# Kernel optimization log

Measured on AMD Instinct MI355X. Metric: run time of the kernel, lower is better.

The kernel has to match this reference:

```python
import jax, jax.numpy as jnp
import numpy as np

H = 1024; W = 1024
SPACE_SIGMA = 16.0; RANGE_SIGMA = 0.25
PAD_XY = 2; PAD_Z = 2
DIM = 5


def setup_inputs() -> dict:
    key = jax.random.key(0)
    k1, k2 = jax.random.split(key)
    features = jax.random.uniform(k1, (H, W, 3), dtype=jnp.float32)
    inp = jax.random.normal(k2, (H, W, 3), dtype=jnp.float32)
    return {"features": features, "inp": inp}


def _grid_dims(features_np):
    # Grid sizes are data-dependent in the original (TF builds them from
    # per-channel min/max); compute them host-side from concrete inputs.
    sh = int(float(H - 1) / SPACE_SIGMA) + 1 + 2 * PAD_XY
    sw = int(float(W - 1) / SPACE_SIGMA) + 1 + 2 * PAD_XY
    depths = []
    for c in range(3):
        ch = features_np[..., c]
        delta = float(ch.max() - ch.min())
        depths.append(int(delta / RANGE_SIGMA) + 1 + 2 * PAD_Z)
    return (sh, sw, depths[0], depths[1], depths[2])


def _both_indices(size, coord):
    left = jnp.clip(coord.astype(jnp.int32), 0, size - 1)
    right = jnp.clip(left + 1, 0, size - 1)
    return left, right


def _convn(data, n_iter=2):
    # Faithful port of the TF convn: separable [1,2,1]/4 pass per axis with
    # the exact same ping-pong buffer / boundary-keep / transpose behavior.
    buffer = jnp.zeros_like(data)
    perm = (1, 2, 3, 4, 0)
    for _ in range(n_iter):
        buffer, data = data, buffer
        for _ in range(DIM):
            newdata = (buffer[:-2] + buffer[2:] + 2.0 * buffer[1:-1]) / 4.0
            data = jnp.concatenate([data[:1], newdata, data[-1:]], axis=0)
            data = jnp.transpose(data, perm)
            buffer = jnp.transpose(buffer, perm)
    return data


def _filter(features, inp, dims):
    sh, sw, dr, dg, db = dims
    hw = H * W
    yy, xx = jnp.meshgrid(jnp.arange(H, dtype=jnp.float32),
                          jnp.arange(W, dtype=jnp.float32), indexing="ij")
    splat_yy = (yy / SPACE_SIGMA + 0.5).astype(jnp.int32) + PAD_XY
    splat_xx = (xx / SPACE_SIGMA + 0.5).astype(jnp.int32) + PAD_XY
    slice_yy = yy / SPACE_SIGMA + PAD_XY
    slice_xx = xx / SPACE_SIGMA + PAD_XY
    y_i, y_i2 = _both_indices(sh, slice_yy)
    x_i, x_i2 = _both_indices(sw, slice_xx)
    y_alpha = (slice_yy - y_i.astype(jnp.float32)).reshape(-1)
    x_alpha = (slice_xx - x_i.astype(jnp.float32)).reshape(-1)

    chans = []
    for c, depth in zip(range(3), (dr, dg, db)):
        v = features[..., c]
        v0 = v - jnp.min(v)
        splat_v = (v0 / RANGE_SIGMA + 0.5).astype(jnp.int32) + PAD_Z
        slice_v = v0 / RANGE_SIGMA + PAD_Z
        li, ri = _both_indices(depth, slice_v)
        alpha = (slice_v - li.astype(jnp.float32)).reshape(-1)
        chans.append((splat_v, li, ri, alpha))
    (splat_rr, r_i, r_i2, r_alpha) = chans[0]
    (splat_gg, g_i, g_i2, g_alpha) = chans[1]
    (splat_bb, b_i, b_i2, b_alpha) = chans[2]

    splat_coords = ((((splat_yy * sw + splat_xx) * dr + splat_rr) * dg
                     + splat_gg) * db + splat_bb).reshape(-1)  # [hw]

    idx_all = jnp.stack([y_i, y_i2, x_i, x_i2, r_i, r_i2,
                         g_i, g_i2, b_i, b_i2]).reshape(10, hw)
    alphas_all = jnp.stack([1.0 - y_alpha, y_alpha, 1.0 - x_alpha, x_alpha,
                            1.0 - r_alpha, r_alpha, 1.0 - g_alpha, g_alpha,
                            1.0 - b_alpha, b_alpha])  # [10, hw]

    # 32 corners of the 5-D hypercube; sel[c, d] picks left/right index per dim.
    corners = np.stack(np.meshgrid(*([np.arange(2)] * DIM), indexing="ij"),
                       axis=-1).reshape(-1, DIM)
    sel = corners + np.arange(DIM) * 2  # [32, 5]

    strides = (sw, dr, dg, db)
    coord = idx_all[sel[:, 0]]  # [32, hw]
    for d in range(1, DIM):
        coord = coord * strides[d - 1] + idx_all[sel[:, d]]
    alpha_prod = alphas_all[sel[:, 0]]  # [32, hw]
    for d in range(1, DIM):
        alpha_prod = alpha_prod * alphas_all[sel[:, d]]

    total = sh * sw * dr * dg * db

    def ch_filter(ch):
        grid = jnp.zeros((total,), jnp.float32).at[splat_coords].add(ch.reshape(-1))
        grid = _convn(grid.reshape(sh, sw, dr, dg, db))
        vals = grid.reshape(-1)[coord]  # [32, hw] multilinear gather
        return jnp.sum(alpha_prod * vals, axis=0).reshape(H, W)

    outT = jax.vmap(ch_filter)(jnp.transpose(inp, (2, 0, 1)))
    return jnp.transpose(outT, (1, 2, 0))


def reference(features, inp):
    dims = _grid_dims(np.asarray(features))
    return _filter(features, inp, dims)
```

## Files before the change

kernel.cpp:

```cpp
#include <hip/hip_runtime.h>

namespace {

constexpr int kH  = 1024;
constexpr int kW  = 1024;
constexpr int kHW = kH * kW;
constexpr int kSH = 68;
constexpr int kSW = 68;
constexpr int kD  = 8;
constexpr int kT3 = kSH * kSW * kD * kD * kD;

__global__ void minmax_kernel(const float* __restrict__ feat, float* __restrict__ part) {
    const float4* f4 = (const float4*)feat;
    float mn[3] = {1e30f, 1e30f, 1e30f};
    float mx[3] = {-1e30f, -1e30f, -1e30f};
    int tid = blockIdx.x * blockDim.x + threadIdx.x;
    int stride = gridDim.x * blockDim.x;
    for (int c = tid; c < kHW / 4; c += stride) {
        float4 q0 = f4[c * 3], q1 = f4[c * 3 + 1], q2 = f4[c * 3 + 2];
        mn[0] = fminf(mn[0], fminf(fminf(q0.x, q0.w), fminf(q1.z, q2.y)));
        mx[0] = fmaxf(mx[0], fmaxf(fmaxf(q0.x, q0.w), fmaxf(q1.z, q2.y)));
        mn[1] = fminf(mn[1], fminf(fminf(q0.y, q1.x), fminf(q1.w, q2.z)));
        mx[1] = fmaxf(mx[1], fmaxf(fmaxf(q0.y, q1.x), fmaxf(q1.w, q2.z)));
        mn[2] = fminf(mn[2], fminf(fminf(q0.z, q1.y), fminf(q2.x, q2.w)));
        mx[2] = fmaxf(mx[2], fmaxf(fmaxf(q0.z, q1.y), fmaxf(q2.x, q2.w)));
    }
    #pragma unroll
    for (int off = 32; off > 0; off >>= 1) {
        #pragma unroll
        for (int c = 0; c < 3; ++c) {
            mn[c] = fminf(mn[c], __shfl_down(mn[c], off, 64));
            mx[c] = fmaxf(mx[c], __shfl_down(mx[c], off, 64));
        }
    }
    __shared__ float smn[4][3], smx[4][3];
    int wave = threadIdx.x >> 6;
    if ((threadIdx.x & 63) == 0) {
        #pragma unroll
        for (int c = 0; c < 3; ++c) { smn[wave][c] = mn[c]; smx[wave][c] = mx[c]; }
    }
    __syncthreads();
    if (threadIdx.x == 0) {
        #pragma unroll
        for (int c = 0; c < 3; ++c) {
            part[blockIdx.x * 6 + c]     = fminf(fminf(smn[0][c], smn[1][c]), fminf(smn[2][c], smn[3][c]));
            part[blockIdx.x * 6 + 3 + c] = fmaxf(fmaxf(smx[0][c], smx[1][c]), fmaxf(smx[2][c], smx[3][c]));
        }
    }
}

__global__ void params_kernel(const float* __restrict__ part, float* __restrict__ hdrF) {
    int t = threadIdx.x;
    float mn[3], mx[3];
    #pragma unroll
    for (int c = 0; c < 3; ++c) { mn[c] = part[t * 6 + c]; mx[c] = part[t * 6 + 3 + c]; }
    #pragma unroll
    for (int off = 32; off > 0; off >>= 1) {
        #pragma unroll
        for (int c = 0; c < 3; ++c) {
            mn[c] = fminf(mn[c], __shfl_down(mn[c], off, 64));
            mx[c] = fmaxf(mx[c], __shfl_down(mx[c], off, 64));
        }
    }
    __shared__ float smn[4][3], smx[4][3];
    int wave = t >> 6;
    if ((t & 63) == 0) {
        #pragma unroll
        for (int c = 0; c < 3; ++c) { smn[wave][c] = mn[c]; smx[wave][c] = mx[c]; }
    }
    __syncthreads();
    if (t == 0) {
        int* ip = (int*)(hdrF + 8);
        #pragma unroll
        for (int c = 0; c < 3; ++c) {
            float bmn = fminf(fminf(smn[0][c], smn[1][c]), fminf(smn[2][c], smn[3][c]));
            float bmx = fmaxf(fmaxf(smx[0][c], smx[1][c]), fmaxf(smx[2][c], smx[3][c]));
            float delta = bmx - bmn;
            int depth = (int)((double)delta / 0.25) + 1 + 4;
            if (depth > kD) depth = kD;
            if (depth < 1) depth = 1;
            hdrF[c] = bmn;
            ip[c] = depth;
        }
    }
}

__global__ __launch_bounds__(256) void splat_kernel(const float* __restrict__ feat,
                                                    const float* __restrict__ inp,
                                                    const float* __restrict__ hdrF,
                                                    float* __restrict__ grid) {
    int ix = blockIdx.x, iy = blockIdx.y;
    int y0 = (iy == 0) ? 0 : 16 * iy - 8;
    int x0 = (ix == 0) ? 0 : 16 * ix - 8;
    int h = (iy == 0 || iy == 64) ? 8 : 16;
    int w = (ix == 0 || ix == 64) ? 8 : 16;

    __shared__ float acc[3 * 512];
    __shared__ float fS[16 * 48], iS[16 * 48];
    for (int i = threadIdx.x; i < 3 * 512; i += 256) acc[i] = 0.0f;

    int rowVec = (w * 3) >> 2;
    int nvec = h * rowVec;
    const float4* f4 = (const float4*)(feat + ((long)y0 * kW + x0) * 3);
    const float4* i4 = (const float4*)(inp  + ((long)y0 * kW + x0) * 3);
    for (int t = threadIdx.x; t < nvec; t += 256) {
        int row = t / rowVec, q = t - row * rowVec;
        ((float4*)fS)[row * rowVec + q] = f4[row * (kW * 3 / 4) + q];
        ((float4*)iS)[row * rowVec + q] = i4[row * (kW * 3 / 4) + q];
    }
    __syncthreads();

    int t = threadIdx.x;
    int n = w * h;
    if (t < n) {
        int lx = t & (w - 1);
        int ly = (w == 16) ? (t >> 4) : (t >> 3);
        int o = (ly * w + lx) * 3;
        float v0 = fS[o + 0] - hdrF[0];
        float v1 = fS[o + 1] - hdrF[1];
        float v2 = fS[o + 2] - hdrF[2];
        int sr = (int)(v0 * 4.0f + 0.5f) + 2;
        int sg = (int)(v1 * 4.0f + 0.5f) + 2;
        int sb = (int)(v2 * 4.0f + 0.5f) + 2;
        int ci = (sr << 6) + (sg << 3) + sb;
        atomicAdd(&acc[ci],        iS[o + 0]);
        atomicAdd(&acc[512 + ci],  iS[o + 1]);
        atomicAdd(&acc[1024 + ci], iS[o + 2]);
    }
    __syncthreads();

    long base = ((long)((iy + 2) * kSW + (ix + 2))) << 9;
    for (int i = threadIdx.x; i < 512; i += 256) {
        int b = i >> 6, r = (i >> 3) & 7, g = i & 7;
        int s = (r << 6) + (g << 3) + b;
        grid[base + i]            = acc[s];
        grid[kT3 + base + i]      = acc[512 + s];
        grid[2 * kT3 + base + i]  = acc[1024 + s];
    }
}

__global__ __launch_bounds__(192) void blur2_kernel(float* __restrict__ dst,
                                                    const float* __restrict__ src,
                                                    const float* __restrict__ hdrF) {
    int cx = blockIdx.x + 2, cy = blockIdx.y + 2;
    const int* ip = (const int*)(hdrF + 8);
    int dr = ip[0], dg = ip[1], db = ip[2];

    __shared__ float Sv[3 * 576];
    long cbase = ((long)(cy * kSW + cx)) << 9;

    {
        const float4* g4 = (const float4*)src;
        for (int i = threadIdx.x; i < 384; i += 192) {
            int ch = i >> 7, i4 = i & 127;
            float4 q = g4[(long)ch * (kT3 / 4) + (cbase >> 2) + i4];
            int b = i4 >> 4;
            int rg = ((i4 >> 1) & 7) * 8 + (i4 & 1) * 4;
            *(float4*)&Sv[ch * 576 + b * 72 + rg] = q;
        }
    }
    __syncthreads();

    int ch = threadIdx.x >> 6;
    int rg = threadIdx.x & 63;
    int r = rg >> 3, g = rg & 7;

    float* S = Sv + ch * 576;
    auto SV = [&](int b, int l) -> float { return S[b * 72 + l]; };
    auto gsp = [&](int ccy, int ccx, int rr, int gg, int bb) -> float {
        if (ccy < 2 || ccy > 66 || ccx < 2 || ccx > 66) return 0.0f;
        return src[(long)ch * kT3 + (((long)(ccy * kSW + ccx)) << 9) + (bb << 6) + (rr << 3) + gg];
    };

    bool gI = (g >= 1) && (g <= dg - 2);
    bool rI = (r >= 1) && (r <= dr - 2);

    float v[8];
    #pragma unroll
    for (int b = 0; b < 8; ++b) v[b] = SV(b, rg);

    int eHi = db - 1;

    auto o1_end = [&](int e) -> float {
        float Vm, Vp;
        if (gI)      { Vm = SV(e, rg - 1); Vp = SV(e, rg + 1); }
        else if (rI) { Vm = SV(e, rg - 8); Vp = SV(e, rg + 8); }
        else         { Vm = gsp(cy, cx - 1, r, g, e); Vp = gsp(cy, cx + 1, r, g, e); }
        return (Vm + Vp + 2.0f * SV(e, rg)) * 0.25f;
    };
    float o1_lo = o1_end(0);
    float o1_hi = o1_end(eHi);

    float o1[8];
    #pragma unroll
    for (int b = 0; b < 8; ++b) {
        float iv = 0.0f;
        if (b >= 1 && b <= 6) iv = ((v[b - 1] + v[b + 1]) + 2.0f * v[b]) * 0.25f;
        o1[b] = (b >= 1 && b <= db - 2) ? iv : (b == 0 ? o1_lo : (b == eHi ? o1_hi : 0.0f));
    }

    auto out1_in = [&](int r2, int g2, int e) -> float {
        int l2 = (r2 << 3) + g2;
        float C = SV(e, l2);
        float Nm, Np;
        if (g2 >= 1 && g2 <= dg - 2)      { Nm = SV(e, l2 - 1); Np = SV(e, l2 + 1); }
        else if (r2 >= 1 && r2 <= dr - 2) { Nm = SV(e, l2 - 8); Np = SV(e, l2 + 8); }
        else { Nm = gsp(cy, cx - 1, r2, g2, e); Np = gsp(cy, cx + 1, r2, g2, e); }
        return (Nm + Np + 2.0f * C) * 0.25f;
    };
    auto out1_x = [&](int cx2, int e) -> float {
        float C = gsp(cy, cx2, r, g, e);
        float Nm, Np;
        if (cx2 >= 1 && cx2 <= kSW - 2) { Nm = gsp(cy, cx2 - 1, r, g, e); Np = gsp(cy, cx2 + 1, r, g, e); }
        else                            { Nm = gsp(cy - 1, cx2, r, g, e); Np = gsp(cy + 1, cx2, r, g, e); }
        return (Nm + Np + 2.0f * C) * 0.25f;
    };
    auto o2_end = [&](int e, float o1e) -> float {
        float Xm, Xp;
        if (gI)      { Xm = out1_in(r, g - 1, e); Xp = out1_in(r, g + 1, e); }
        else if (rI) { Xm = out1_in(r - 1, g, e); Xp = out1_in(r + 1, g, e); }
        else         { Xm = out1_x(cx - 1, e);    Xp = out1_x(cx + 1, e); }
        return (Xm + Xp + 2.0f * o1e) * 0.25f;
    };
    float o2_lo = o2_end(0, o1_lo);
    float o2_hi = o2_end(eHi, o1_hi);

    float o2[8];
    #pragma unroll
    for (int b = 0; b < 8; ++b) {
        float iv = 0.0f;
        if (b >= 1 && b <= 6) iv = ((o1[b - 1] + o1[b + 1]) + 2.0f * o1[b]) * 0.25f;
        o2[b] = (b >= 1 && b <= db - 2) ? iv : (b == 0 ? o2_lo : (b == eHi ? o2_hi : 0.0f));
    }

    float* dp = dst + (long)ch * kT3 + cbase + (rg << 3);
    *(float4*)dp       = make_float4(o2[0], o2[1], o2[2], o2[3]);
    *(float4*)(dp + 4) = make_float4(o2[4], o2[5], o2[6], o2[7]);
}

__global__ __launch_bounds__(256) void slice_kernel(const float* __restrict__ feat,
                                                    const float* __restrict__ hdrF,
                                                    const float* __restrict__ grid,
                                                    float* __restrict__ out) {
    __shared__ float sg[3 * 4 * 512 + 8];
    int tx = blockIdx.x, ty = blockIdx.y;

    {
        const float4* g4 = (const float4*)grid;
        float4* s4 = (float4*)sg;
        #pragma unroll
        for (int it = 0; it < 2; ++it) {
            int i = threadIdx.x + it * 256;
            int cell = i >> 7;
            int ci4 = i & 127;
            int cy = ty + 2 + (cell >> 1), cx = tx + 2 + (cell & 1);
            long cbase4 = ((long)(cy * kSW + cx)) << 7;
            #pragma unroll
            for (int ch = 0; ch < 3; ++ch)
                s4[ch * 512 + i] = g4[(long)ch * (kT3 / 4) + cbase4 + ci4];
        }
    }
    __syncthreads();

    const int* ip = (const int*)(hdrF + 8);
    int d3[3] = {ip[0], ip[1], ip[2]};
    int lx = threadIdx.x & 15, ly = threadIdx.x >> 4;
    int y = (ty << 4) + ly, x = (tx << 4) + lx;
    int p = (y << 10) + x;

    float ya = (float)ly * 0.0625f;
    float xa = (float)lx * 0.0625f;

    int li[3], ri[3];
    float al[3];
    #pragma unroll
    for (int c = 0; c < 3; ++c) {
        float v0 = feat[p * 3 + c] - hdrF[c];
        float sv = v0 * 4.0f + 2.0f;
        int l = (int)sv;
        int dm = d3[c] - 1;
        l = l < 0 ? 0 : (l > dm ? dm : l);
        int rr = l + 1 > dm ? dm : l + 1;
        li[c] = l; ri[c] = rr; al[c] = sv - (float)l;
    }

    float spw[4];
    {
        float wy[2] = {1.0f - ya, ya};
        float wx[2] = {1.0f - xa, xa};
        spw[0] = wy[0] * wx[0]; spw[1] = wy[0] * wx[1];
        spw[2] = wy[1] * wx[0]; spw[3] = wy[1] * wx[1];
    }
    int rs[2] = {li[0], ri[0]}; float wrr[2] = {1.0f - al[0], al[0]};
    int gs[2] = {li[1], ri[1]}; float wgg[2] = {1.0f - al[1], al[1]};
    int bq = li[2];
    float aeff = (ri[2] > li[2]) ? al[2] : 0.0f;

    float acc0 = 0.0f, acc1 = 0.0f, acc2 = 0.0f;
    #pragma unroll
    for (int k = 0; k < 4; ++k) {
        #pragma unroll
        for (int cr = 0; cr < 2; ++cr)
        #pragma unroll
        for (int cg = 0; cg < 2; ++cg) {
            int si = (k << 9) + (rs[cr] << 6) + (gs[cg] << 3) + bq;
            float w = spw[k] * wrr[cr] * wgg[cg];
            float a0 = sg[si],        a1 = sg[si + 1];
            float b0 = sg[2048 + si], b1 = sg[2048 + si + 1];
            float c0 = sg[4096 + si], c1 = sg[4096 + si + 1];
            acc0 += w * (a0 + aeff * (a1 - a0));
            acc1 += w * (b0 + aeff * (b1 - b0));
            acc2 += w * (c0 + aeff * (c1 - c0));
        }
    }
    out[p * 3 + 0] = acc0;
    out[p * 3 + 1] = acc1;
    out[p * 3 + 2] = acc2;
}

}

extern "C" void kernel_launch(void* const* d_in, const int* in_sizes, int n_in,
                              void* d_out, int out_size, void* d_ws, size_t ws_size,
                              hipStream_t stream) {
    const float* feat = (const float*)d_in[0];
    const float* inp  = (const float*)d_in[1];
    float* out = (float*)d_out;

    float* hdrF  = (float*)d_ws;
    float* part  = (float*)((char*)d_ws + 1024);
    float* gridA = (float*)((char*)d_ws + 8192);
    float* gridB = gridA + 3 * (size_t)kT3;

    minmax_kernel<<<256, 256, 0, stream>>>(feat, part);
    params_kernel<<<1, 256, 0, stream>>>(part, hdrF);

    splat_kernel<<<dim3(65, 65), 256, 0, stream>>>(feat, inp, hdrF, gridA);
    blur2_kernel<<<dim3(65, 65), 192, 0, stream>>>(gridB, gridA, hdrF);
    slice_kernel<<<dim3(64, 64), 256, 0, stream>>>(feat, hdrF, gridB, out);
}
```

Baseline: 142.7 us.

## Fuse blur into slice kernel, recomputing blurred cells per tile

Removes the separate blur kernel and its intermediate grid buffer. The slice kernel now loads the raw splatted grid for its 2x2 cell neighborhood into shared memory, blurs those cells in place (with global fallbacks for boundary neighbors), writes the results back to shared memory, then slices. This saves one launch and a full grid write/read, at the cost of redundant blur work, since each cell is blurred by up to four tiles, plus more register pressure.

```diff
diff --git a/kernel.cpp b/kernel.cpp
--- a/kernel.cpp
+++ b/kernel.cpp
@@ -139,109 +139,10 @@
     }
 }
 
-__global__ __launch_bounds__(192) void blur2_kernel(float* __restrict__ dst,
-                                                    const float* __restrict__ src,
-                                                    const float* __restrict__ hdrF) {
-    int cx = blockIdx.x + 2, cy = blockIdx.y + 2;
-    const int* ip = (const int*)(hdrF + 8);
-    int dr = ip[0], dg = ip[1], db = ip[2];
-
-    __shared__ float Sv[3 * 576];
-    long cbase = ((long)(cy * kSW + cx)) << 9;
-
-    {
-        const float4* g4 = (const float4*)src;
-        for (int i = threadIdx.x; i < 384; i += 192) {
-            int ch = i >> 7, i4 = i & 127;
-            float4 q = g4[(long)ch * (kT3 / 4) + (cbase >> 2) + i4];
-            int b = i4 >> 4;
-            int rg = ((i4 >> 1) & 7) * 8 + (i4 & 1) * 4;
-            *(float4*)&Sv[ch * 576 + b * 72 + rg] = q;
-        }
-    }
-    __syncthreads();
-
-    int ch = threadIdx.x >> 6;
-    int rg = threadIdx.x & 63;
-    int r = rg >> 3, g = rg & 7;
-
-    float* S = Sv + ch * 576;
-    auto SV = [&](int b, int l) -> float { return S[b * 72 + l]; };
-    auto gsp = [&](int ccy, int ccx, int rr, int gg, int bb) -> float {
-        if (ccy < 2 || ccy > 66 || ccx < 2 || ccx > 66) return 0.0f;
-        return src[(long)ch * kT3 + (((long)(ccy * kSW + ccx)) << 9) + (bb << 6) + (rr << 3) + gg];
-    };
-
-    bool gI = (g >= 1) && (g <= dg - 2);
-    bool rI = (r >= 1) && (r <= dr - 2);
-
-    float v[8];
-    #pragma unroll
-    for (int b = 0; b < 8; ++b) v[b] = SV(b, rg);
-
-    int eHi = db - 1;
-
-    auto o1_end = [&](int e) -> float {
-        float Vm, Vp;
-        if (gI)      { Vm = SV(e, rg - 1); Vp = SV(e, rg + 1); }
-        else if (rI) { Vm = SV(e, rg - 8); Vp = SV(e, rg + 8); }
-        else         { Vm = gsp(cy, cx - 1, r, g, e); Vp = gsp(cy, cx + 1, r, g, e); }
-        return (Vm + Vp + 2.0f * SV(e, rg)) * 0.25f;
-    };
-    float o1_lo = o1_end(0);
-    float o1_hi = o1_end(eHi);
-
-    float o1[8];
-    #pragma unroll
-    for (int b = 0; b < 8; ++b) {
-        float iv = 0.0f;
-        if (b >= 1 && b <= 6) iv = ((v[b - 1] + v[b + 1]) + 2.0f * v[b]) * 0.25f;
-        o1[b] = (b >= 1 && b <= db - 2) ? iv : (b == 0 ? o1_lo : (b == eHi ? o1_hi : 0.0f));
-    }
-
-    auto out1_in = [&](int r2, int g2, int e) -> float {
-        int l2 = (r2 << 3) + g2;
-        float C = SV(e, l2);
-        float Nm, Np;
-        if (g2 >= 1 && g2 <= dg - 2)      { Nm = SV(e, l2 - 1); Np = SV(e, l2 + 1); }
-        else if (r2 >= 1 && r2 <= dr - 2) { Nm = SV(e, l2 - 8); Np = SV(e, l2 + 8); }
-        else { Nm = gsp(cy, cx - 1, r2, g2, e); Np = gsp(cy, cx + 1, r2, g2, e); }
-        return (Nm + Np + 2.0f * C) * 0.25f;
-    };
-    auto out1_x = [&](int cx2, int e) -> float {
-        float C = gsp(cy, cx2, r, g, e);
-        float Nm, Np;
-        if (cx2 >= 1 && cx2 <= kSW - 2) { Nm = gsp(cy, cx2 - 1, r, g, e); Np = gsp(cy, cx2 + 1, r, g, e); }
-        else                            { Nm = gsp(cy - 1, cx2, r, g, e); Np = gsp(cy + 1, cx2, r, g, e); }
-        return (Nm + Np + 2.0f * C) * 0.25f;
-    };
-    auto o2_end = [&](int e, float o1e) -> float {
-        float Xm, Xp;
-        if (gI)      { Xm = out1_in(r, g - 1, e); Xp = out1_in(r, g + 1, e); }
-        else if (rI) { Xm = out1_in(r - 1, g, e); Xp = out1_in(r + 1, g, e); }
-        else         { Xm = out1_x(cx - 1, e);    Xp = out1_x(cx + 1, e); }
-        return (Xm + Xp + 2.0f * o1e) * 0.25f;
-    };
-    float o2_lo = o2_end(0, o1_lo);
-    float o2_hi = o2_end(eHi, o1_hi);
-
-    float o2[8];
-    #pragma unroll
-    for (int b = 0; b < 8; ++b) {
-        float iv = 0.0f;
-        if (b >= 1 && b <= 6) iv = ((o1[b - 1] + o1[b + 1]) + 2.0f * o1[b]) * 0.25f;
-        o2[b] = (b >= 1 && b <= db - 2) ? iv : (b == 0 ? o2_lo : (b == eHi ? o2_hi : 0.0f));
-    }
-
-    float* dp = dst + (long)ch * kT3 + cbase + (rg << 3);
-    *(float4*)dp       = make_float4(o2[0], o2[1], o2[2], o2[3]);
-    *(float4*)(dp + 4) = make_float4(o2[4], o2[5], o2[6], o2[7]);
-}
-
-__global__ __launch_bounds__(256) void slice_kernel(const float* __restrict__ feat,
-                                                    const float* __restrict__ hdrF,
-                                                    const float* __restrict__ grid,
-                                                    float* __restrict__ out) {
+__global__ __launch_bounds__(256) void blurslice_kernel(const float* __restrict__ feat,
+                                                        const float* __restrict__ hdrF,
+                                                        const float* __restrict__ grid,
+                                                        float* __restrict__ out) {
     __shared__ float sg[3 * 4 * 512 + 8];
     int tx = blockIdx.x, ty = blockIdx.y;
 
@@ -263,7 +164,93 @@
     __syncthreads();
 
     const int* ip = (const int*)(hdrF + 8);
-    int d3[3] = {ip[0], ip[1], ip[2]};
+    int dr = ip[0], dg = ip[1], db = ip[2];
+
+    int cell = threadIdx.x >> 6;
+    int rg = threadIdx.x & 63;
+    int r = rg >> 3, g = rg & 7;
+    int cy = ty + 2 + (cell >> 1), cx = tx + 2 + (cell & 1);
+
+    bool gI = (g >= 1) && (g <= dg - 2);
+    bool rI = (r >= 1) && (r <= dr - 2);
+    int eHi = db - 1;
+
+    float o2all[3][8];
+    #pragma unroll
+    for (int ch = 0; ch < 3; ++ch) {
+        float* S = sg + (ch * 4 + cell) * 512;
+        auto SV = [&](int b, int l) -> float { return S[(b << 6) + l]; };
+        auto gsp = [&](int ccy, int ccx, int rr, int gg, int bb) -> float {
+            if (ccy < 2 || ccy > 66 || ccx < 2 || ccx > 66) return 0.0f;
+            return grid[(long)ch * kT3 + (((long)(ccy * kSW + ccx)) << 9) + (bb << 6) + (rr << 3) + gg];
+        };
+
+        float v[8];
+        #pragma unroll
+        for (int b = 0; b < 8; ++b) v[b] = SV(b, rg);
+
+        auto o1_end = [&](int e) -> float {
+            float Vm, Vp;
+            if (gI)      { Vm = SV(e, rg - 1); Vp = SV(e, rg + 1); }
+            else if (rI) { Vm = SV(e, rg - 8); Vp = SV(e, rg + 8); }
+            else         { Vm = gsp(cy, cx - 1, r, g, e); Vp = gsp(cy, cx + 1, r, g, e); }
+            return (Vm + Vp + 2.0f * SV(e, rg)) * 0.25f;
+        };
+        float o1_lo = o1_end(0);
+        float o1_hi = o1_end(eHi);
+
+        float o1[8];
+        #pragma unroll
+        for (int b = 0; b < 8; ++b) {
+            float iv = 0.0f;
+            if (b >= 1 && b <= 6) iv = ((v[b - 1] + v[b + 1]) + 2.0f * v[b]) * 0.25f;
+            o1[b] = (b >= 1 && b <= db - 2) ? iv : (b == 0 ? o1_lo : (b == eHi ? o1_hi : 0.0f));
+        }
+
+        auto out1_in = [&](int r2, int g2, int e) -> float {
+            int l2 = (r2 << 3) + g2;
+            float C = SV(e, l2);
+            float Nm, Np;
+            if (g2 >= 1 && g2 <= dg - 2)      { Nm = SV(e, l2 - 1); Np = SV(e, l2 + 1); }
+            else if (r2 >= 1 && r2 <= dr - 2) { Nm = SV(e, l2 - 8); Np = SV(e, l2 + 8); }
+            else { Nm = gsp(cy, cx - 1, r2, g2, e); Np = gsp(cy, cx + 1, r2, g2, e); }
+            return (Nm + Np + 2.0f * C) * 0.25f;
+        };
+        auto out1_x = [&](int cx2, int e) -> float {
+            float C = gsp(cy, cx2, r, g, e);
+            float Nm, Np;
+            if (cx2 >= 1 && cx2 <= kSW - 2) { Nm = gsp(cy, cx2 - 1, r, g, e); Np = gsp(cy, cx2 + 1, r, g, e); }
+            else                            { Nm = gsp(cy - 1, cx2, r, g, e); Np = gsp(cy + 1, cx2, r, g, e); }
+            return (Nm + Np + 2.0f * C) * 0.25f;
+        };
+        auto o2_end = [&](int e, float o1e) -> float {
+            float Xm, Xp;
+            if (gI)      { Xm = out1_in(r, g - 1, e); Xp = out1_in(r, g + 1, e); }
+            else if (rI) { Xm = out1_in(r - 1, g, e); Xp = out1_in(r + 1, g, e); }
+            else         { Xm = out1_x(cx - 1, e);    Xp = out1_x(cx + 1, e); }
+            return (Xm + Xp + 2.0f * o1e) * 0.25f;
+        };
+        float o2_lo = o2_end(0, o1_lo);
+        float o2_hi = o2_end(eHi, o1_hi);
+
+        #pragma unroll
+        for (int b = 0; b < 8; ++b) {
+            float iv = 0.0f;
+            if (b >= 1 && b <= 6) iv = ((o1[b - 1] + o1[b + 1]) + 2.0f * o1[b]) * 0.25f;
+            o2all[ch][b] = (b >= 1 && b <= db - 2) ? iv : (b == 0 ? o2_lo : (b == eHi ? o2_hi : 0.0f));
+        }
+    }
+    __syncthreads();
+
+    #pragma unroll
+    for (int ch = 0; ch < 3; ++ch) {
+        float* dp = sg + (ch * 4 + cell) * 512 + (rg << 3);
+        *(float4*)dp       = make_float4(o2all[ch][0], o2all[ch][1], o2all[ch][2], o2all[ch][3]);
+        *(float4*)(dp + 4) = make_float4(o2all[ch][4], o2all[ch][5], o2all[ch][6], o2all[ch][7]);
+    }
+    __syncthreads();
+
+    int d3[3] = {dr, dg, db};
     int lx = threadIdx.x & 15, ly = threadIdx.x >> 4;
     int y = (ty << 4) + ly, x = (tx << 4) + lx;
     int p = (y << 10) + x;
@@ -330,12 +317,10 @@
     float* hdrF  = (float*)d_ws;
     float* part  = (float*)((char*)d_ws + 1024);
     float* gridA = (float*)((char*)d_ws + 8192);
-    float* gridB = gridA + 3 * (size_t)kT3;
 
     minmax_kernel<<<256, 256, 0, stream>>>(feat, part);
     params_kernel<<<1, 256, 0, stream>>>(part, hdrF);
 
     splat_kernel<<<dim3(65, 65), 256, 0, stream>>>(feat, inp, hdrF, gridA);
-    blur2_kernel<<<dim3(65, 65), 192, 0, stream>>>(gridB, gridA, hdrF);
-    slice_kernel<<<dim3(64, 64), 256, 0, stream>>>(feat, hdrF, gridB, out);
-}
+    blurslice_kernel<<<dim3(64, 64), 256, 0, stream>>>(feat, hdrF, gridA, out);
+}
```

Measured after the change: 179.8 us. 1.26x slower.

## Fuse params reduction into splat kernel and specialize blur for full depth

Applied to the files above, without the earlier changes.

Removes the single-block params kernel launch by having every splat block redundantly reduce the 256 min/max partials itself, with block (0,0) writing the header for later kernels. Splat now loads its features and inputs straight into registers instead of staging them through shared memory, and issues those loads before the reduction so their latency overlaps it. The blur kernel gains a templated body with a constant-depth path for depths of 8. The costs are redundant reduction work in each of the 4225 splat blocks and uncoalesced stride-3 global loads in splat.

```diff
diff --git a/kernel.cpp b/kernel.cpp
--- a/kernel.cpp
+++ b/kernel.cpp
@@ -49,7 +49,9 @@
     }
 }
 
-__global__ void params_kernel(const float* __restrict__ part, float* __restrict__ hdrF) {
+__device__ __forceinline__ void reduce_params(const float* __restrict__ part,
+                                              float mnout[3], int dout[3],
+                                              float* sred ) {
     int t = threadIdx.x;
     float mn[3], mx[3];
     #pragma unroll
@@ -62,70 +64,70 @@
             mx[c] = fmaxf(mx[c], __shfl_down(mx[c], off, 64));
         }
     }
-    __shared__ float smn[4][3], smx[4][3];
-    int wave = t >> 6;
     if ((t & 63) == 0) {
-        #pragma unroll
-        for (int c = 0; c < 3; ++c) { smn[wave][c] = mn[c]; smx[wave][c] = mx[c]; }
-    }
-    __syncthreads();
-    if (t == 0) {
-        int* ip = (int*)(hdrF + 8);
-        #pragma unroll
-        for (int c = 0; c < 3; ++c) {
-            float bmn = fminf(fminf(smn[0][c], smn[1][c]), fminf(smn[2][c], smn[3][c]));
-            float bmx = fmaxf(fmaxf(smx[0][c], smx[1][c]), fmaxf(smx[2][c], smx[3][c]));
-            float delta = bmx - bmn;
-            int depth = (int)((double)delta / 0.25) + 1 + 4;
-            if (depth > kD) depth = kD;
-            if (depth < 1) depth = 1;
-            hdrF[c] = bmn;
-            ip[c] = depth;
-        }
+        int w = t >> 6;
+        #pragma unroll
+        for (int c = 0; c < 3; ++c) { sred[w * 6 + c] = mn[c]; sred[w * 6 + 3 + c] = mx[c]; }
+    }
+    __syncthreads();
+    #pragma unroll
+    for (int c = 0; c < 3; ++c) {
+        float bmn = fminf(fminf(sred[c], sred[6 + c]), fminf(sred[12 + c], sred[18 + c]));
+        float bmx = fmaxf(fmaxf(sred[3 + c], sred[9 + c]), fmaxf(sred[15 + c], sred[21 + c]));
+        float delta = bmx - bmn;
+        int depth = (int)((double)delta / 0.25) + 1 + 4;
+        if (depth > kD) depth = kD;
+        if (depth < 1) depth = 1;
+        mnout[c] = bmn;
+        dout[c] = depth;
     }
 }
 
 __global__ __launch_bounds__(256) void splat_kernel(const float* __restrict__ feat,
                                                     const float* __restrict__ inp,
-                                                    const float* __restrict__ hdrF,
-                                                    float* __restrict__ grid) {
+                                                    const float* __restrict__ part,
+                                                    float* __restrict__ grid,
+                                                    float* __restrict__ hdrF) {
     int ix = blockIdx.x, iy = blockIdx.y;
     int y0 = (iy == 0) ? 0 : 16 * iy - 8;
     int x0 = (ix == 0) ? 0 : 16 * ix - 8;
     int h = (iy == 0 || iy == 64) ? 8 : 16;
     int w = (ix == 0 || ix == 64) ? 8 : 16;
 
+    __shared__ float sred[24];
     __shared__ float acc[3 * 512];
-    __shared__ float fS[16 * 48], iS[16 * 48];
-    for (int i = threadIdx.x; i < 3 * 512; i += 256) acc[i] = 0.0f;
-
-    int rowVec = (w * 3) >> 2;
-    int nvec = h * rowVec;
-    const float4* f4 = (const float4*)(feat + ((long)y0 * kW + x0) * 3);
-    const float4* i4 = (const float4*)(inp  + ((long)y0 * kW + x0) * 3);
-    for (int t = threadIdx.x; t < nvec; t += 256) {
-        int row = t / rowVec, q = t - row * rowVec;
-        ((float4*)fS)[row * rowVec + q] = f4[row * (kW * 3 / 4) + q];
-        ((float4*)iS)[row * rowVec + q] = i4[row * (kW * 3 / 4) + q];
-    }
-    __syncthreads();
 
     int t = threadIdx.x;
     int n = w * h;
-    if (t < n) {
+    bool act = t < n;
+    float f0 = 0, f1 = 0, f2 = 0, v0 = 0, v1 = 0, v2 = 0;
+    if (act) {
         int lx = t & (w - 1);
         int ly = (w == 16) ? (t >> 4) : (t >> 3);
-        int o = (ly * w + lx) * 3;
-        float v0 = fS[o + 0] - hdrF[0];
-        float v1 = fS[o + 1] - hdrF[1];
-        float v2 = fS[o + 2] - hdrF[2];
-        int sr = (int)(v0 * 4.0f + 0.5f) + 2;
-        int sg = (int)(v1 * 4.0f + 0.5f) + 2;
-        int sb = (int)(v2 * 4.0f + 0.5f) + 2;
+        long p = ((long)(y0 + ly) * kW + (x0 + lx)) * 3;
+        f0 = feat[p];     f1 = feat[p + 1]; f2 = feat[p + 2];
+        v0 = inp[p];      v1 = inp[p + 1];  v2 = inp[p + 2];
+    }
+
+    for (int i = threadIdx.x; i < 3 * 512; i += 256) acc[i] = 0.0f;
+
+    float mn3[3]; int d3[3];
+    reduce_params(part, mn3, d3, sred);
+
+    if (ix == 0 && iy == 0 && t == 0) {
+        int* ip = (int*)(hdrF + 8);
+        #pragma unroll
+        for (int c = 0; c < 3; ++c) { hdrF[c] = mn3[c]; ip[c] = d3[c]; }
+    }
+
+    if (act) {
+        int sr = (int)((f0 - mn3[0]) * 4.0f + 0.5f) + 2;
+        int sg = (int)((f1 - mn3[1]) * 4.0f + 0.5f) + 2;
+        int sb = (int)((f2 - mn3[2]) * 4.0f + 0.5f) + 2;
         int ci = (sr << 6) + (sg << 3) + sb;
-        atomicAdd(&acc[ci],        iS[o + 0]);
-        atomicAdd(&acc[512 + ci],  iS[o + 1]);
-        atomicAdd(&acc[1024 + ci], iS[o + 2]);
+        atomicAdd(&acc[ci],        v0);
+        atomicAdd(&acc[512 + ci],  v1);
+        atomicAdd(&acc[1024 + ci], v2);
     }
     __syncthreads();
 
@@ -137,6 +139,89 @@
         grid[kT3 + base + i]      = acc[512 + s];
         grid[2 * kT3 + base + i]  = acc[1024 + s];
     }
+}
+
+template <bool FAST>
+__device__ __forceinline__ void blur_body(float* __restrict__ dst,
+                                          const float* __restrict__ src,
+                                          const float* __restrict__ Sv,
+                                          int cx, int cy, long cbase,
+                                          int dr, int dg, int db) {
+    int ch = threadIdx.x >> 6;
+    int rg = threadIdx.x & 63;
+    int r = rg >> 3, g = rg & 7;
+
+    const float* S = Sv + ch * 576;
+    auto SV = [&](int b, int l) -> float { return S[b * 72 + l]; };
+    auto gsp = [&](int ccy, int ccx, int rr, int gg, int bb) -> float {
+        if (ccy < 2 || ccy > 66 || ccx < 2 || ccx > 66) return 0.0f;
+        return src[(long)ch * kT3 + (((long)(ccy * kSW + ccx)) << 9) + (bb << 6) + (rr << 3) + gg];
+    };
+
+    bool gI = (g >= 1) && (g <= dg - 2);
+    bool rI = (r >= 1) && (r <= dr - 2);
+
+    float v[8];
+    #pragma unroll
+    for (int b = 0; b < 8; ++b) v[b] = SV(b, rg);
+
+    int eHi = db - 1;
+
+    auto o1_end = [&](int e) -> float {
+        float Vm, Vp;
+        if (gI)      { Vm = SV(e, rg - 1); Vp = SV(e, rg + 1); }
+        else if (rI) { Vm = SV(e, rg - 8); Vp = SV(e, rg + 8); }
+        else         { Vm = gsp(cy, cx - 1, r, g, e); Vp = gsp(cy, cx + 1, r, g, e); }
+        return (Vm + Vp + 2.0f * SV(e, rg)) * 0.25f;
+    };
+    float o1_lo = o1_end(0);
+    float o1_hi = o1_end(eHi);
+
+    float o1[8];
+    #pragma unroll
+    for (int b = 0; b < 8; ++b) {
+        float iv = 0.0f;
+        if (b >= 1 && b <= 6) iv = ((v[b - 1] + v[b + 1]) + 2.0f * v[b]) * 0.25f;
+        o1[b] = (b >= 1 && b <= db - 2) ? iv : (b == 0 ? o1_lo : (b == eHi ? o1_hi : 0.0f));
+    }
+
+    auto out1_in = [&](int r2, int g2, int e) -> float {
+        int l2 = (r2 << 3) + g2;
+        float C = SV(e, l2);
+        float Nm, Np;
+        if (g2 >= 1 && g2 <= dg - 2)      { Nm = SV(e, l2 - 1); Np = SV(e, l2 + 1); }
+        else if (r2 >= 1 && r2 <= dr - 2) { Nm = SV(e, l2 - 8); Np = SV(e, l2 + 8); }
+        else { Nm = gsp(cy, cx - 1, r2, g2, e); Np = gsp(cy, cx + 1, r2, g2, e); }
+        return (Nm + Np + 2.0f * C) * 0.25f;
+    };
+    auto out1_x = [&](int cx2, int e) -> float {
+        float C = gsp(cy, cx2, r, g, e);
+        float Nm, Np;
+        if (cx2 >= 1 && cx2 <= kSW - 2) { Nm = gsp(cy, cx2 - 1, r, g, e); Np = gsp(cy, cx2 + 1, r, g, e); }
+        else                            { Nm = gsp(cy - 1, cx2, r, g, e); Np = gsp(cy + 1, cx2, r, g, e); }
+        return (Nm + Np + 2.0f * C) * 0.25f;
+    };
+    auto o2_end = [&](int e, float o1e) -> float {
+        float Xm, Xp;
+        if (gI)      { Xm = out1_in(r, g - 1, e); Xp = out1_in(r, g + 1, e); }
+        else if (rI) { Xm = out1_in(r - 1, g, e); Xp = out1_in(r + 1, g, e); }
+        else         { Xm = out1_x(cx - 1, e);    Xp = out1_x(cx + 1, e); }
+        return (Xm + Xp + 2.0f * o1e) * 0.25f;
+    };
+    float o2_lo = o2_end(0, o1_lo);
+    float o2_hi = o2_end(eHi, o1_hi);
+
+    float o2[8];
+    #pragma unroll
+    for (int b = 0; b < 8; ++b) {
+        float iv = 0.0f;
+        if (b >= 1 && b <= 6) iv = ((o1[b - 1] + o1[b + 1]) + 2.0f * o1[b]) * 0.25f;
+        o2[b] = (b >= 1 && b <= db - 2) ? iv : (b == 0 ? o2_lo : (b == eHi ? o2_hi : 0.0f));
+    }
+
+    float* dp = dst + (long)ch * kT3 + cbase + (rg << 3);
+    *(float4*)dp       = make_float4(o2[0], o2[1], o2[2], o2[3]);
+    *(float4*)(dp + 4) = make_float4(o2[4], o2[5], o2[6], o2[7]);
 }
 
 __global__ __launch_bounds__(192) void blur2_kernel(float* __restrict__ dst,
@@ -161,81 +246,11 @@
     }
     __syncthreads();
 
-    int ch = threadIdx.x >> 6;
-    int rg = threadIdx.x & 63;
-    int r = rg >> 3, g = rg & 7;
-
-    float* S = Sv + ch * 576;
-    auto SV = [&](int b, int l) -> float { return S[b * 72 + l]; };
-    auto gsp = [&](int ccy, int ccx, int rr, int gg, int bb) -> float {
-        if (ccy < 2 || ccy > 66 || ccx < 2 || ccx > 66) return 0.0f;
-        return src[(long)ch * kT3 + (((long)(ccy * kSW + ccx)) << 9) + (bb << 6) + (rr << 3) + gg];
-    };
-
-    bool gI = (g >= 1) && (g <= dg - 2);
-    bool rI = (r >= 1) && (r <= dr - 2);
-
-    float v[8];
-    #pragma unroll
-    for (int b = 0; b < 8; ++b) v[b] = SV(b, rg);
-
-    int eHi = db - 1;
-
-    auto o1_end = [&](int e) -> float {
-        float Vm, Vp;
-        if (gI)      { Vm = SV(e, rg - 1); Vp = SV(e, rg + 1); }
-        else if (rI) { Vm = SV(e, rg - 8); Vp = SV(e, rg + 8); }
-        else         { Vm = gsp(cy, cx - 1, r, g, e); Vp = gsp(cy, cx + 1, r, g, e); }
-        return (Vm + Vp + 2.0f * SV(e, rg)) * 0.25f;
-    };
-    float o1_lo = o1_end(0);
-    float o1_hi = o1_end(eHi);
-
-    float o1[8];
-    #pragma unroll
-    for (int b = 0; b < 8; ++b) {
-        float iv = 0.0f;
-        if (b >= 1 && b <= 6) iv = ((v[b - 1] + v[b + 1]) + 2.0f * v[b]) * 0.25f;
-        o1[b] = (b >= 1 && b <= db - 2) ? iv : (b == 0 ? o1_lo : (b == eHi ? o1_hi : 0.0f));
-    }
-
-    auto out1_in = [&](int r2, int g2, int e) -> float {
-        int l2 = (r2 << 3) + g2;
-        float C = SV(e, l2);
-        float Nm, Np;
-        if (g2 >= 1 && g2 <= dg - 2)      { Nm = SV(e, l2 - 1); Np = SV(e, l2 + 1); }
-        else if (r2 >= 1 && r2 <= dr - 2) { Nm = SV(e, l2 - 8); Np = SV(e, l2 + 8); }
-        else { Nm = gsp(cy, cx - 1, r2, g2, e); Np = gsp(cy, cx + 1, r2, g2, e); }
-        return (Nm + Np + 2.0f * C) * 0.25f;
-    };
-    auto out1_x = [&](int cx2, int e) -> float {
-        float C = gsp(cy, cx2, r, g, e);
-        float Nm, Np;
-        if (cx2 >= 1 && cx2 <= kSW - 2) { Nm = gsp(cy, cx2 - 1, r, g, e); Np = gsp(cy, cx2 + 1, r, g, e); }
-        else                            { Nm = gsp(cy - 1, cx2, r, g, e); Np = gsp(cy + 1, cx2, r, g, e); }
-        return (Nm + Np + 2.0f * C) * 0.25f;
-    };
-    auto o2_end = [&](int e, float o1e) -> float {
-        float Xm, Xp;
-        if (gI)      { Xm = out1_in(r, g - 1, e); Xp = out1_in(r, g + 1, e); }
-        else if (rI) { Xm = out1_in(r - 1, g, e); Xp = out1_in(r + 1, g, e); }
-        else         { Xm = out1_x(cx - 1, e);    Xp = out1_x(cx + 1, e); }
-        return (Xm + Xp + 2.0f * o1e) * 0.25f;
-    };
-    float o2_lo = o2_end(0, o1_lo);
-    float o2_hi = o2_end(eHi, o1_hi);
-
-    float o2[8];
-    #pragma unroll
-    for (int b = 0; b < 8; ++b) {
-        float iv = 0.0f;
-        if (b >= 1 && b <= 6) iv = ((o1[b - 1] + o1[b + 1]) + 2.0f * o1[b]) * 0.25f;
-        o2[b] = (b >= 1 && b <= db - 2) ? iv : (b == 0 ? o2_lo : (b == eHi ? o2_hi : 0.0f));
-    }
-
-    float* dp = dst + (long)ch * kT3 + cbase + (rg << 3);
-    *(float4*)dp       = make_float4(o2[0], o2[1], o2[2], o2[3]);
-    *(float4*)(dp + 4) = make_float4(o2[4], o2[5], o2[6], o2[7]);
+    if (dr == 8 && dg == 8 && db == 8) {
+        blur_body<true>(dst, src, Sv, cx, cy, cbase, 8, 8, 8);
+    } else {
+        blur_body<false>(dst, src, Sv, cx, cy, cbase, dr, dg, db);
+    }
 }
 
 __global__ __launch_bounds__(256) void slice_kernel(const float* __restrict__ feat,
@@ -333,9 +348,7 @@
     float* gridB = gridA + 3 * (size_t)kT3;
 
     minmax_kernel<<<256, 256, 0, stream>>>(feat, part);
-    params_kernel<<<1, 256, 0, stream>>>(part, hdrF);
-
-    splat_kernel<<<dim3(65, 65), 256, 0, stream>>>(feat, inp, hdrF, gridA);
+    splat_kernel<<<dim3(65, 65), 256, 0, stream>>>(feat, inp, part, gridA, hdrF);
     blur2_kernel<<<dim3(65, 65), 192, 0, stream>>>(gridB, gridA, hdrF);
     slice_kernel<<<dim3(64, 64), 256, 0, stream>>>(feat, hdrF, gridB, out);
 }
```

New measurement: 148.1 us. 3.8% more time.
